# Kernel tuning notes

Measured on AMD Instinct MI355X. Metric: run time of the kernel, lower is better.

## Reference

```python
import jax, jax.numpy as jnp
import numpy as np

D_MODEL, DFF, OUT, SEQ = 256, 1024, 32, 512
SIGMA = 0.1          # sigma for q/k/v/z SMC noise
SIGMA_OBS = 0.5      # observation noise


def _layernorm(x, g, b, eps=1e-6):
    mu = jnp.mean(x, axis=-1, keepdims=True)
    var = jnp.mean(jnp.square(x - mu), axis=-1, keepdims=True)
    return (x - mu) * jax.lax.rsqrt(var + eps) * g + b


def _resample(params, i_t, t):
    # params: (B,P,S,D); i_t: (B,P) ancestor indices; resample only the past [:t+1]
    past = jnp.take_along_axis(params[:, :, :t + 1, :], i_t[:, :, None, None], axis=1)
    return jnp.concatenate([past, params[:, :, t + 1:, :]], axis=2)


def setup_inputs() -> dict:
    key = jax.random.key(0)
    ks = jax.random.split(key, 24)
    B, P = 32, 10
    d = {
        'x': jax.random.normal(ks[0], (B, P, D_MODEL), jnp.float32),
        'y': jax.random.normal(ks[1], (B, P, OUT), jnp.float32),
        'K': jax.random.normal(ks[2], (B, P, SEQ, D_MODEL), jnp.float32),
        'V': jax.random.normal(ks[3], (B, P, SEQ, D_MODEL), jnp.float32),
        'R': jax.random.normal(ks[4], (B, P, SEQ, D_MODEL), jnp.float32),
        'noise_q': jax.random.normal(ks[5], (B, P, 1, D_MODEL), jnp.float32),
        'noise_k': jax.random.normal(ks[6], (B, P, 1, D_MODEL), jnp.float32),
        'noise_v': jax.random.normal(ks[7], (B, P, 1, D_MODEL), jnp.float32),
        'noise_z': jax.random.normal(ks[8], (B, P, 1, D_MODEL), jnp.float32),
        'dec_timestep': 256,
    }
    s = 0.02
    d['wq_w'] = jax.random.normal(ks[9], (D_MODEL, D_MODEL), jnp.float32) * s
    d['wq_b'] = jnp.zeros((D_MODEL,), jnp.float32)
    d['wk_w'] = jax.random.normal(ks[10], (D_MODEL, D_MODEL), jnp.float32) * s
    d['wk_b'] = jnp.zeros((D_MODEL,), jnp.float32)
    d['wv_w'] = jax.random.normal(ks[11], (D_MODEL, D_MODEL), jnp.float32) * s
    d['wv_b'] = jnp.zeros((D_MODEL,), jnp.float32)
    d['wz_w'] = jax.random.normal(ks[12], (D_MODEL, D_MODEL), jnp.float32) * s
    d['wz_b'] = jnp.zeros((D_MODEL,), jnp.float32)
    d['ln1_g'] = jnp.ones((D_MODEL,), jnp.float32)
    d['ln1_b'] = jnp.zeros((D_MODEL,), jnp.float32)
    d['ffn_w1'] = jax.random.normal(ks[13], (D_MODEL, DFF), jnp.float32) * s
    d['ffn_b1'] = jnp.zeros((DFF,), jnp.float32)
    d['ffn_w2'] = jax.random.normal(ks[14], (DFF, D_MODEL), jnp.float32) * s
    d['ffn_b2'] = jnp.zeros((D_MODEL,), jnp.float32)
    d['ln2_g'] = jnp.ones((D_MODEL,), jnp.float32)
    d['ln2_b'] = jnp.zeros((D_MODEL,), jnp.float32)
    d['out_w'] = jax.random.normal(ks[15], (D_MODEL, OUT), jnp.float32) * s
    d['out_b'] = jnp.zeros((OUT,), jnp.float32)
    return d


def reference(x, y, K, V, R, noise_q, noise_k, noise_v, noise_z,
              wq_w, wq_b, wk_w, wk_b, wv_w, wv_b, wz_w, wz_b,
              ln1_g, ln1_b, ffn_w1, ffn_b1, ffn_w2, ffn_b2,
              ln2_g, ln2_b, out_w, out_b, dec_timestep):
    t = dec_timestep
    B, P, D = x.shape
    sq = jnp.sqrt(jnp.float32(SIGMA))
    xq = x[:, :, None, :]           # (B,P,1,D)
    yq = y[:, :, None, :]           # (B,P,1,F_y)
    # --- Self_Attention_SMC: project current token, add SMC gaussian noise ---
    q = xq @ wq_w + wq_b + sq * noise_q
    k = xq @ wk_w + wk_b + sq * noise_k
    v = xq @ wv_w + wv_b + sq * noise_v
    # in-place style KV cache update at timestep t (concat past/new/future)
    K = jnp.concatenate([K[:, :, :t, :], k, K[:, :, t + 1:, :]], axis=2)
    V = jnp.concatenate([V[:, :, :t, :], v, V[:, :, t + 1:, :]], axis=2)
    logits = jnp.einsum('bpod,bpsd->bpos', q, K) / jnp.sqrt(jnp.float32(D))
    attn_weights = jax.nn.softmax(logits, axis=-1)          # (B,P,1,S)
    z = jnp.einsum('bpos,bpsd->bpod', attn_weights, V)
    z = z @ wz_w + wz_b + sq * noise_z
    # --- full_model: layernorm + FFN + layernorm ---
    out = _layernorm(z + xq, ln1_g, ln1_b)
    r = jax.nn.relu(out @ ffn_w1 + ffn_b1) @ ffn_w2 + ffn_b2
    r = _layernorm(r + out, ln2_g, ln2_b)                   # (B,P,1,D)
    predictions = r @ out_w + out_b                          # (B,P,1,F_y)
    R = jnp.concatenate([R[:, :, :t, :], r, R[:, :, t + 1:, :]], axis=2)
    mu = jnp.squeeze(yq - predictions, axis=-2)              # (B,P,F_y)
    log_w = -jnp.sum(mu * mu, axis=-1) / (2.0 * SIGMA_OBS)   # (B,P)
    w = jax.nn.softmax(jnp.exp(log_w), axis=-1)              # faithful to original (softmax of exp)
    w = jax.lax.stop_gradient(w)
    # categorical resampling of ancestors (tf.random.categorical uses w as logits)
    i_t = jax.random.categorical(jax.random.key(42), w[:, None, :], shape=(B, P))
    i_t = jax.lax.stop_gradient(i_t)
    K = _resample(K, i_t, t)
    V = _resample(V, i_t, t)
    R = _resample(R, i_t, t)
    return r, attn_weights, K, V, R, w
```

## Files before the change

kernel.cpp:

```cpp
#include <hip/hip_runtime.h>
#include <hip/hip_bf16.h>
#include <stdint.h>

#define BATCH 32
#define NPART 10
#define BP_TOT 320
#define DM 256
#define FF 1024
#define OD 32
#define SL 512

#define SQRT_SIGMA 0.31622776601683794f

__device__ __forceinline__ uint32_t rotl32(uint32_t x, uint32_t r) {
    return (x << r) | (x >> (32u - r));
}

__device__ __forceinline__ void threefry2x32(uint32_t k0, uint32_t k1,
                                             uint32_t x0, uint32_t x1,
                                             uint32_t& o0, uint32_t& o1) {
    uint32_t k2 = k0 ^ k1 ^ 0x1BD11BDAu;
    uint32_t x = x0 + k0, y = x1 + k1;
#define TFR(r) { x += y; y = rotl32(y, r); y ^= x; }
    TFR(13u) TFR(15u) TFR(26u) TFR(6u)
    x += k1; y += k2 + 1u;
    TFR(17u) TFR(29u) TFR(16u) TFR(24u)
    x += k2; y += k0 + 2u;
    TFR(13u) TFR(15u) TFR(26u) TFR(6u)
    x += k0; y += k1 + 3u;
    TFR(17u) TFR(29u) TFR(16u) TFR(24u)
    x += k1; y += k2 + 4u;
    TFR(13u) TFR(15u) TFR(26u) TFR(6u)
    x += k2; y += k0 + 5u;
#undef TFR
    o0 = x; o1 = y;
}

__device__ __forceinline__ float jax_gumbel_part(uint32_t m) {
    const float TINY = 1.17549435e-38f;
    uint32_t o0, o1;
    threefry2x32(0u, 42u, 0u, m, o0, o1);
    uint32_t bits = o0 ^ o1;
    uint32_t fb = (bits >> 9) | 0x3f800000u;
    float f = __uint_as_float(fb) - 1.0f;
    float u = fmaxf(TINY, f + TINY);
    return -logf(-logf(u));
}

__global__ __launch_bounds__(256) void qkv_kernel(
    const float* __restrict__ x,
    const float* __restrict__ nq, const float* __restrict__ nk,
    const float* __restrict__ nv,
    const float* __restrict__ wq_w, const float* __restrict__ wq_b,
    const float* __restrict__ wk_w, const float* __restrict__ wk_b,
    const float* __restrict__ wv_w, const float* __restrict__ wv_b,
    float* __restrict__ qtmp, float* __restrict__ knew, float* __restrict__ vnew)
{
    const int bp = blockIdx.x;
    const int m  = blockIdx.y;
    const int d  = threadIdx.x;

    __shared__ float xs[DM];
    xs[d] = x[bp * DM + d];
    __syncthreads();

    const float* W; const float* bias; const float* noise; float* outp;
    if (m == 0)      { W = wq_w; bias = wq_b; noise = nq; outp = qtmp + (size_t)bp * SL; }
    else if (m == 1) { W = wk_w; bias = wk_b; noise = nk; outp = knew + (size_t)bp * DM; }
    else             { W = wv_w; bias = wv_b; noise = nv; outp = vnew + (size_t)bp * DM; }

    float a0 = 0.f, a1 = 0.f, a2 = 0.f, a3 = 0.f;
    #pragma unroll 4
    for (int i = 0; i < 64; ++i) {
        a0 = fmaf(xs[i],       W[(i      ) * DM + d], a0);
        a1 = fmaf(xs[i +  64], W[(i +  64) * DM + d], a1);
        a2 = fmaf(xs[i + 128], W[(i + 128) * DM + d], a2);
        a3 = fmaf(xs[i + 192], W[(i + 192) * DM + d], a3);
    }
    outp[d] = (a0 + a1) + (a2 + a3) + bias[d] + SQRT_SIGMA * noise[bp * DM + d];
}

__global__ __launch_bounds__(256) void attn_chunk_kernel(
    const float* __restrict__ Kin, const float* __restrict__ Vin,
    const float* __restrict__ knew, const float* __restrict__ vnew,
    const float* __restrict__ qtmp, const int* __restrict__ t_ptr,
    float* __restrict__ Kout, float* __restrict__ Vout,
    float* __restrict__ logits, float* __restrict__ zpart,
    float* __restrict__ mstat)
{
    const int bp   = blockIdx.x;
    const int sc   = blockIdx.y;
    const int tid  = threadIdx.x;
    const int lane = tid & 63;
    const int wave = tid >> 6;
    const int t    = *t_ptr;

    __shared__ float qs[DM], ks[DM], vs[DM];
    __shared__ float att_loc[128];
    __shared__ float scratch[4 * 256];
    __shared__ float redm[2], rede[2];

    if (tid < DM) {
        qs[tid] = qtmp[(size_t)bp * SL + tid];
        ks[tid] = knew[(size_t)bp * DM + tid];
        vs[tid] = vnew[(size_t)bp * DM + tid];
    }
    __syncthreads();

    const float* Kbp = Kin + (size_t)bp * SL * DM;
    const float* Vbp = Vin + (size_t)bp * SL * DM;
    float4 q4 = *(const float4*)&qs[lane * 4];
    const int s0 = sc * 128 + wave * 32;

    for (int j0 = 0; j0 < 32; j0 += 8) {
        float4 k4[8];
        #pragma unroll
        for (int u = 0; u < 8; ++u) {
            int s = s0 + j0 + u;
            k4[u] = (s == t) ? *(const float4*)&ks[lane * 4]
                             : *(const float4*)&Kbp[(size_t)s * DM + lane * 4];
        }
        #pragma unroll
        for (int u = 0; u < 8; ++u) {
            int s = s0 + j0 + u;
            if (s > t) *(float4*)(Kout + ((size_t)bp * SL + s) * DM + lane * 4) = k4[u];
            float acc = q4.x * k4[u].x + q4.y * k4[u].y + q4.z * k4[u].z + q4.w * k4[u].w;
            #pragma unroll
            for (int off = 32; off; off >>= 1) acc += __shfl_down(acc, off);
            if (lane == 0) {
                float l = acc * 0.0625f;
                att_loc[wave * 32 + j0 + u] = l;
                logits[(size_t)bp * SL + s] = l;
            }
        }
    }
    __syncthreads();

    float l = (tid < 128) ? att_loc[tid] : -3.402823466e+38f;
    float mm = l;
    #pragma unroll
    for (int off = 32; off; off >>= 1) mm = fmaxf(mm, __shfl_down(mm, off));
    if (tid < 128 && lane == 0) redm[wave] = mm;
    __syncthreads();
    const float m_loc = fmaxf(redm[0], redm[1]);
    float p = (tid < 128) ? expf(l - m_loc) : 0.f;
    if (tid < 128) att_loc[tid] = p;
    float e = p;
    #pragma unroll
    for (int off = 32; off; off >>= 1) e += __shfl_down(e, off);
    if (tid < 128 && lane == 0) rede[wave] = e;
    __syncthreads();
    const float e_loc = rede[0] + rede[1];

    float4 z4 = make_float4(0.f, 0.f, 0.f, 0.f);
    for (int j0 = 0; j0 < 32; j0 += 8) {
        float4 v4[8];
        #pragma unroll
        for (int u = 0; u < 8; ++u) {
            int s = s0 + j0 + u;
            v4[u] = (s == t) ? *(const float4*)&vs[lane * 4]
                             : *(const float4*)&Vbp[(size_t)s * DM + lane * 4];
        }
        #pragma unroll
        for (int u = 0; u < 8; ++u) {
            int s = s0 + j0 + u;
            if (s > t) *(float4*)(Vout + ((size_t)bp * SL + s) * DM + lane * 4) = v4[u];
            float a = att_loc[wave * 32 + j0 + u];
            z4.x = fmaf(a, v4[u].x, z4.x);
            z4.y = fmaf(a, v4[u].y, z4.y);
            z4.z = fmaf(a, v4[u].z, z4.z);
            z4.w = fmaf(a, v4[u].w, z4.w);
        }
    }
    *(float4*)&scratch[wave * 256 + lane * 4] = z4;
    __syncthreads();
    if (tid < DM) {
        float zp = (scratch[tid] + scratch[256 + tid]) + (scratch[512 + tid] + scratch[768 + tid]);
        zpart[((size_t)bp * 4 + sc) * DM + tid] = zp;
    }
    if (tid == 0) {
        mstat[((size_t)bp * 4 + sc) * 2 + 0] = m_loc;
        mstat[((size_t)bp * 4 + sc) * 2 + 1] = e_loc;
    }
}

__global__ __launch_bounds__(256) void attn_combine_kernel(
    const float* __restrict__ logits, const float* __restrict__ zpart,
    const float* __restrict__ mstat,
    float* __restrict__ attn_out, float* __restrict__ ztmp)
{
    const int bp  = blockIdx.x;
    const int tid = threadIdx.x;

    const float* ms = mstat + (size_t)bp * 8;
    float m0 = ms[0], e0 = ms[1], m1 = ms[2], e1 = ms[3];
    float m2 = ms[4], e2 = ms[5], m3 = ms[6], e3 = ms[7];
    float gm = fmaxf(fmaxf(m0, m1), fmaxf(m2, m3));
    float f0 = expf(m0 - gm), f1 = expf(m1 - gm);
    float f2 = expf(m2 - gm), f3 = expf(m3 - gm);
    float inv = 1.0f / (e0 * f0 + e1 * f1 + e2 * f2 + e3 * f3);

    float l0 = logits[(size_t)bp * SL + tid];
    float l1 = logits[(size_t)bp * SL + tid + 256];
    attn_out[(size_t)bp * SL + tid]       = expf(l0 - gm) * inv;
    attn_out[(size_t)bp * SL + tid + 256] = expf(l1 - gm) * inv;

    const float* zp = zpart + (size_t)bp * 4 * DM;
    float z = (zp[tid] * f0 + zp[DM + tid] * f1)
            + (zp[2 * DM + tid] * f2 + zp[3 * DM + tid] * f3);
    ztmp[(size_t)bp * DM + tid] = z * inv;
}

__global__ __launch_bounds__(1024) void post_kernel(
    const float* __restrict__ x, const float* __restrict__ nz,
    const float* __restrict__ wz_w, const float* __restrict__ wz_b,
    const float* __restrict__ ln1_g, const float* __restrict__ ln1_b,
    const float* __restrict__ w1, const float* __restrict__ b1,
    const float* __restrict__ w2, const float* __restrict__ b2,
    const float* __restrict__ ln2_g, const float* __restrict__ ln2_b,
    float* __restrict__ r_out)
{
    const int bp   = blockIdx.x;
    const int tid  = threadIdx.x;
    const int lane = tid & 63;
    const int wave = tid >> 6;
    const int grp  = tid >> 8;
    const int qtid = tid & 255;

    __shared__ float buf[DM];
    __shared__ float xs[DM];
    __shared__ float hid[FF];
    __shared__ float scratch[1024];
    __shared__ float red[32];

    if (tid < DM) {
        buf[tid] = r_out[(size_t)bp * DM + tid];
        xs[tid]  = x[bp * DM + tid];
    }
    __syncthreads();

    {
        const int i0 = grp * 64;
        float a0 = 0.f, a1 = 0.f;
        #pragma unroll 4
        for (int ii = 0; ii < 32; ++ii) {
            a0 = fmaf(buf[i0 + ii],      wz_w[(i0 + ii)      * DM + qtid], a0);
            a1 = fmaf(buf[i0 + ii + 32], wz_w[(i0 + ii + 32) * DM + qtid], a1);
        }
        scratch[grp * 256 + qtid] = a0 + a1;
    }
    __syncthreads();
    float h = 0.f;
    if (tid < DM) {
        float az = (scratch[tid] + scratch[256 + tid]) + (scratch[512 + tid] + scratch[768 + tid]);
        h = az + wz_b[tid] + SQRT_SIGMA * nz[bp * DM + tid] + xs[tid];
    }

    float s1 = h;
    #pragma unroll
    for (int off = 32; off; off >>= 1) s1 += __shfl_down(s1, off);
    if (lane == 0) red[wave] = s1;
    __syncthreads();
    float mu = (red[0] + red[1] + red[2] + red[3]) * (1.0f / DM);
    float dv = (tid < DM) ? (h - mu) : 0.f;
    float s2 = dv * dv;
    #pragma unroll
    for (int off = 32; off; off >>= 1) s2 += __shfl_down(s2, off);
    if (lane == 0) red[16 + wave] = s2;
    __syncthreads();
    float var = (red[16] + red[17] + red[18] + red[19]) * (1.0f / DM);
    float o = 0.f;
    __syncthreads();
    if (tid < DM) {
        o = dv * rsqrtf(var + 1e-6f) * ln1_g[tid] + ln1_b[tid];
        buf[tid] = o;
    }
    __syncthreads();

    {
        float h0 = 0.f, h1 = 0.f, h2 = 0.f, h3 = 0.f;
        #pragma unroll 4
        for (int i = 0; i < 64; ++i) {
            h0 = fmaf(buf[i],       w1[(i      ) * FF + tid], h0);
            h1 = fmaf(buf[i +  64], w1[(i +  64) * FF + tid], h1);
            h2 = fmaf(buf[i + 128], w1[(i + 128) * FF + tid], h2);
            h3 = fmaf(buf[i + 192], w1[(i + 192) * FF + tid], h3);
        }
        hid[tid] = fmaxf((h0 + h1) + (h2 + h3) + b1[tid], 0.f);
    }
    __syncthreads();

    {
        const int i0 = grp * 256;
        float a0 = 0.f, a1 = 0.f, a2 = 0.f, a3 = 0.f;
        #pragma unroll 4
        for (int ii = 0; ii < 64; ++ii) {
            a0 = fmaf(hid[i0 + ii],       w2[(i0 + ii      ) * DM + qtid], a0);
            a1 = fmaf(hid[i0 + ii +  64], w2[(i0 + ii +  64) * DM + qtid], a1);
            a2 = fmaf(hid[i0 + ii + 128], w2[(i0 + ii + 128) * DM + qtid], a2);
            a3 = fmaf(hid[i0 + ii + 192], w2[(i0 + ii + 192) * DM + qtid], a3);
        }
        scratch[grp * 256 + qtid] = (a0 + a1) + (a2 + a3);
    }
    __syncthreads();
    float rr = 0.f;
    if (tid < DM) {
        rr = (scratch[tid] + scratch[256 + tid]) + (scratch[512 + tid] + scratch[768 + tid])
           + b2[tid] + o;
    }

    float t1 = rr;
    #pragma unroll
    for (int off = 32; off; off >>= 1) t1 += __shfl_down(t1, off);
    if (lane == 0) red[wave] = t1;
    __syncthreads();
    float mu2 = (red[0] + red[1] + red[2] + red[3]) * (1.0f / DM);
    float dv2 = (tid < DM) ? (rr - mu2) : 0.f;
    float t2 = dv2 * dv2;
    #pragma unroll
    for (int off = 32; off; off >>= 1) t2 += __shfl_down(t2, off);
    if (lane == 0) red[16 + wave] = t2;
    __syncthreads();
    float var2 = (red[16] + red[17] + red[18] + red[19]) * (1.0f / DM);
    if (tid < DM) {
        float rf = dv2 * rsqrtf(var2 + 1e-6f) * ln2_g[tid] + ln2_b[tid];
        r_out[(size_t)bp * DM + tid] = rf;
    }
}

__global__ __launch_bounds__(320) void weights_kernel(
    const float* __restrict__ r, const float* __restrict__ y,
    const float* __restrict__ out_w, const float* __restrict__ out_b,
    float* __restrict__ w_out, int* __restrict__ i_t)
{
    const int b   = blockIdx.x;
    const int tid = threadIdx.x;
    const int p   = tid >> 5;
    const int j   = tid & 31;

    __shared__ float sred[NPART];
    __shared__ float es[NPART];
    __shared__ float pe[NPART];
    __shared__ float wsm[NPART];

    const float* rrow = r + (size_t)(b * NPART + p) * DM;
    float acc = 0.f;
    #pragma unroll 4
    for (int i = 0; i < DM; ++i) acc = fmaf(rrow[i], out_w[i * OD + j], acc);
    float pred = acc + out_b[j];
    float muv  = y[(size_t)(b * NPART + p) * OD + j] - pred;
    float s    = muv * muv;
    #pragma unroll
    for (int off = 16; off; off >>= 1) s += __shfl_down(s, off, 32);
    if (j == 0) sred[p] = s;
    __syncthreads();

    if (tid < NPART) es[tid] = expf(-sred[tid]);
    __syncthreads();
    if (tid < NPART) {
        float mx = es[0];
        #pragma unroll
        for (int i = 1; i < NPART; ++i) mx = fmaxf(mx, es[i]);
        pe[tid] = expf(es[tid] - mx);
    }
    __syncthreads();
    if (tid < NPART) {
        float sum = 0.f;
        #pragma unroll
        for (int i = 0; i < NPART; ++i) sum += pe[i];
        float wv = pe[tid] / sum;
        w_out[b * NPART + tid] = wv;
        wsm[tid] = wv;
    }
    __syncthreads();

    if (tid < NPART) {
        int pp = tid;
        int best = 0;
        float bests = -3.402823466e+38f;
        #pragma unroll
        for (int jj = 0; jj < NPART; ++jj) {
            uint32_t m = (uint32_t)(b * 100 + pp * 10 + jj);
            float score = jax_gumbel_part(m) + wsm[jj];
            if (score > bests) { bests = score; best = jj; }
        }
        i_t[b * NPART + pp] = best;
    }
}

__global__ __launch_bounds__(256) void resample_kernel(
    const float* __restrict__ Kin, const float* __restrict__ Vin,
    const float* __restrict__ Rin,
    const float* __restrict__ knew, const float* __restrict__ vnew,
    const float* __restrict__ rnew,
    const int* __restrict__ i_t, const int* __restrict__ t_ptr,
    float* __restrict__ Kout, float* __restrict__ Vout, float* __restrict__ Rout)
{
    const int t    = *t_ptr;
    const int ysel = blockIdx.y;
    const int tid  = threadIdx.x;
    size_t idx  = (size_t)blockIdx.x * 256 + tid;
    int lane4 = (int)(idx & 63);
    int row   = (int)(idx >> 6);
    int bpi   = row >> 9;
    int s     = row & 511;

    if (ysel != 2 && s > t) return;

    int b     = bpi / NPART;
    int p     = bpi - b * NPART;
    int srcp  = (s <= t) ? i_t[bpi] : p;
    int src_bpi = b * NPART + srcp;

    const float* src;
    if (s == t) {
        const float* nb = (ysel == 1) ? knew : (ysel == 0) ? vnew : rnew;
        src = nb + (size_t)src_bpi * DM;
    } else {
        const float* base = (ysel == 1) ? Kin : (ysel == 0) ? Vin : Rin;
        src = base + ((size_t)src_bpi * SL + s) * DM;
    }
    float* outb = (ysel == 1) ? Kout : (ysel == 0) ? Vout : Rout;
    float4 v4 = *(const float4*)(src + (size_t)lane4 * 4);
    *(float4*)(outb + (size_t)row * DM + (size_t)lane4 * 4) = v4;
}

extern "C" void kernel_launch(void* const* d_in, const int* in_sizes, int n_in,
                              void* d_out, int out_size, void* d_ws, size_t ws_size,
                              hipStream_t stream) {
    const float* x    = (const float*)d_in[0];
    const float* y    = (const float*)d_in[1];
    const float* Kin  = (const float*)d_in[2];
    const float* Vin  = (const float*)d_in[3];
    const float* Rin  = (const float*)d_in[4];
    const float* nq   = (const float*)d_in[5];
    const float* nk   = (const float*)d_in[6];
    const float* nv   = (const float*)d_in[7];
    const float* nz   = (const float*)d_in[8];
    const int*   tptr = (const int*)d_in[9];
    const float* wq_w = (const float*)d_in[10];
    const float* wq_b = (const float*)d_in[11];
    const float* wk_w = (const float*)d_in[12];
    const float* wk_b = (const float*)d_in[13];
    const float* wv_w = (const float*)d_in[14];
    const float* wv_b = (const float*)d_in[15];
    const float* wz_w = (const float*)d_in[16];
    const float* wz_b = (const float*)d_in[17];
    const float* ln1g = (const float*)d_in[18];
    const float* ln1b = (const float*)d_in[19];
    const float* w1   = (const float*)d_in[20];
    const float* b1   = (const float*)d_in[21];
    const float* w2   = (const float*)d_in[22];
    const float* b2   = (const float*)d_in[23];
    const float* ln2g = (const float*)d_in[24];
    const float* ln2b = (const float*)d_in[25];
    const float* outw = (const float*)d_in[26];
    const float* outb = (const float*)d_in[27];

    float* out = (float*)d_out;
    const size_t R_ELEMS    = (size_t)BP_TOT * DM;
    const size_t ATTN_ELEMS = (size_t)BP_TOT * SL;
    const size_t KVR_ELEMS  = (size_t)BP_TOT * SL * DM;
    float* r_out    = out;
    float* attn_out = out + R_ELEMS;
    float* K_out    = out + R_ELEMS + ATTN_ELEMS;
    float* V_out    = K_out + KVR_ELEMS;
    float* R_out    = V_out + KVR_ELEMS;
    float* w_out    = R_out + KVR_ELEMS;

    float* knew = (float*)d_ws;
    float* vnew = knew + R_ELEMS;
    int*   i_t  = (int*)(vnew + R_ELEMS);

    float* logits = R_out;
    float* zpart  = R_out + ATTN_ELEMS;
    float* mstat  = zpart + (size_t)BP_TOT * 4 * DM;

    qkv_kernel<<<dim3(BP_TOT, 3), 256, 0, stream>>>(
        x, nq, nk, nv, wq_w, wq_b, wk_w, wk_b, wv_w, wv_b,
        attn_out, knew, vnew);

    attn_chunk_kernel<<<dim3(BP_TOT, 4), 256, 0, stream>>>(
        Kin, Vin, knew, vnew, attn_out, tptr,
        K_out, V_out, logits, zpart, mstat);

    attn_combine_kernel<<<BP_TOT, 256, 0, stream>>>(
        logits, zpart, mstat, attn_out, r_out);

    post_kernel<<<BP_TOT, 1024, 0, stream>>>(
        x, nz, wz_w, wz_b, ln1g, ln1b, w1, b1, w2, b2, ln2g, ln2b,
        r_out);

    weights_kernel<<<BATCH, 320, 0, stream>>>(
        r_out, y, outw, outb, w_out, i_t);

    resample_kernel<<<dim3(163840 / 4, 3), 256, 0, stream>>>(
        Kin, Vin, Rin, knew, vnew, r_out, i_t, tptr,
        K_out, V_out, R_out);
}
```

Baseline: 337.8 us.

## Batch four particles per block in QKV and post kernels, fuse attention combine

The QKV projection and the post-attention FFN kernels now each handle four particle rows per block, so every weight element loaded from memory feeds four FMAs instead of one. The separate attention-combine kernel is folded into the start of the post kernel, which removes one launch and the round trip of the combined z vector through global memory. Per-thread reductions become longer (full 256- or 1024-deep dot products), and the grids shrink to 80 blocks, which may leave many compute units idle. Shared memory use per block grows as well.

```diff
diff --git a/kernel.cpp b/kernel.cpp
--- a/kernel.cpp
+++ b/kernel.cpp
@@ -56,28 +56,38 @@
     const float* __restrict__ wv_w, const float* __restrict__ wv_b,
     float* __restrict__ qtmp, float* __restrict__ knew, float* __restrict__ vnew)
 {
-    const int bp = blockIdx.x;
+    const int bb = blockIdx.x;
     const int m  = blockIdx.y;
     const int d  = threadIdx.x;
 
-    __shared__ float xs[DM];
-    xs[d] = x[bp * DM + d];
-    __syncthreads();
-
-    const float* W; const float* bias; const float* noise; float* outp;
-    if (m == 0)      { W = wq_w; bias = wq_b; noise = nq; outp = qtmp + (size_t)bp * SL; }
-    else if (m == 1) { W = wk_w; bias = wk_b; noise = nk; outp = knew + (size_t)bp * DM; }
-    else             { W = wv_w; bias = wv_b; noise = nv; outp = vnew + (size_t)bp * DM; }
+    __shared__ float xs[4][DM];
+    #pragma unroll
+    for (int g = 0; g < 4; ++g) xs[g][d] = x[(bb * 4 + g) * DM + d];
+    __syncthreads();
+
+    const float* W; const float* bias; const float* noise;
+    if (m == 0)      { W = wq_w; bias = wq_b; noise = nq; }
+    else if (m == 1) { W = wk_w; bias = wk_b; noise = nk; }
+    else             { W = wv_w; bias = wv_b; noise = nv; }
 
     float a0 = 0.f, a1 = 0.f, a2 = 0.f, a3 = 0.f;
     #pragma unroll 4
-    for (int i = 0; i < 64; ++i) {
-        a0 = fmaf(xs[i],       W[(i      ) * DM + d], a0);
-        a1 = fmaf(xs[i +  64], W[(i +  64) * DM + d], a1);
-        a2 = fmaf(xs[i + 128], W[(i + 128) * DM + d], a2);
-        a3 = fmaf(xs[i + 192], W[(i + 192) * DM + d], a3);
-    }
-    outp[d] = (a0 + a1) + (a2 + a3) + bias[d] + SQRT_SIGMA * noise[bp * DM + d];
+    for (int i = 0; i < DM; ++i) {
+        float wv = W[i * DM + d];
+        a0 = fmaf(xs[0][i], wv, a0);
+        a1 = fmaf(xs[1][i], wv, a1);
+        a2 = fmaf(xs[2][i], wv, a2);
+        a3 = fmaf(xs[3][i], wv, a3);
+    }
+    float r[4] = {a0, a1, a2, a3};
+    #pragma unroll
+    for (int g = 0; g < 4; ++g) {
+        int bp = bb * 4 + g;
+        float v = r[g] + bias[d] + SQRT_SIGMA * noise[bp * DM + d];
+        if (m == 0)      qtmp[(size_t)bp * SL + d] = v;
+        else if (m == 1) knew[(size_t)bp * DM + d] = v;
+        else             vnew[(size_t)bp * DM + d] = v;
+    }
 }
 
 __global__ __launch_bounds__(256) void attn_chunk_kernel(
@@ -184,148 +194,127 @@
     }
 }
 
-__global__ __launch_bounds__(256) void attn_combine_kernel(
+__global__ __launch_bounds__(1024) void post_kernel(
+    const float* __restrict__ x, const float* __restrict__ nz,
     const float* __restrict__ logits, const float* __restrict__ zpart,
     const float* __restrict__ mstat,
-    float* __restrict__ attn_out, float* __restrict__ ztmp)
-{
-    const int bp  = blockIdx.x;
-    const int tid = threadIdx.x;
-
-    const float* ms = mstat + (size_t)bp * 8;
-    float m0 = ms[0], e0 = ms[1], m1 = ms[2], e1 = ms[3];
-    float m2 = ms[4], e2 = ms[5], m3 = ms[6], e3 = ms[7];
-    float gm = fmaxf(fmaxf(m0, m1), fmaxf(m2, m3));
-    float f0 = expf(m0 - gm), f1 = expf(m1 - gm);
-    float f2 = expf(m2 - gm), f3 = expf(m3 - gm);
-    float inv = 1.0f / (e0 * f0 + e1 * f1 + e2 * f2 + e3 * f3);
-
-    float l0 = logits[(size_t)bp * SL + tid];
-    float l1 = logits[(size_t)bp * SL + tid + 256];
-    attn_out[(size_t)bp * SL + tid]       = expf(l0 - gm) * inv;
-    attn_out[(size_t)bp * SL + tid + 256] = expf(l1 - gm) * inv;
-
-    const float* zp = zpart + (size_t)bp * 4 * DM;
-    float z = (zp[tid] * f0 + zp[DM + tid] * f1)
-            + (zp[2 * DM + tid] * f2 + zp[3 * DM + tid] * f3);
-    ztmp[(size_t)bp * DM + tid] = z * inv;
-}
-
-__global__ __launch_bounds__(1024) void post_kernel(
-    const float* __restrict__ x, const float* __restrict__ nz,
     const float* __restrict__ wz_w, const float* __restrict__ wz_b,
     const float* __restrict__ ln1_g, const float* __restrict__ ln1_b,
     const float* __restrict__ w1, const float* __restrict__ b1,
     const float* __restrict__ w2, const float* __restrict__ b2,
     const float* __restrict__ ln2_g, const float* __restrict__ ln2_b,
-    float* __restrict__ r_out)
+    float* __restrict__ attn_out, float* __restrict__ r_out)
 {
-    const int bp   = blockIdx.x;
+    const int bb   = blockIdx.x;
     const int tid  = threadIdx.x;
-    const int lane = tid & 63;
-    const int wave = tid >> 6;
-    const int grp  = tid >> 8;
-    const int qtid = tid & 255;
-
-    __shared__ float buf[DM];
-    __shared__ float xs[DM];
-    __shared__ float hid[FF];
-    __shared__ float scratch[1024];
-    __shared__ float red[32];
-
-    if (tid < DM) {
-        buf[tid] = r_out[(size_t)bp * DM + tid];
-        xs[tid]  = x[bp * DM + tid];
-    }
-    __syncthreads();
+    const int g    = tid >> 8;
+    const int d    = tid & 255;
+    const int wg   = (tid >> 6) & 3;
+    const int bp   = bb * 4 + g;
+
+    __shared__ float bufz[4][DM];
+    __shared__ float xs4[4][DM];
+    __shared__ float hid4[4][FF];
+    __shared__ float part[4][4][DM];
+    __shared__ float red2[4][8];
 
     {
-        const int i0 = grp * 64;
-        float a0 = 0.f, a1 = 0.f;
+        const float* ms = mstat + (size_t)bp * 8;
+        float m0 = ms[0], e0 = ms[1], m1 = ms[2], e1 = ms[3];
+        float m2 = ms[4], e2 = ms[5], m3 = ms[6], e3 = ms[7];
+        float gm = fmaxf(fmaxf(m0, m1), fmaxf(m2, m3));
+        float f0 = expf(m0 - gm), f1 = expf(m1 - gm);
+        float f2 = expf(m2 - gm), f3 = expf(m3 - gm);
+        float inv = 1.0f / (e0 * f0 + e1 * f1 + e2 * f2 + e3 * f3);
+
+        const float* zp = zpart + (size_t)bp * 4 * DM;
+        float z = (zp[d] * f0 + zp[DM + d] * f1)
+                + (zp[2 * DM + d] * f2 + zp[3 * DM + d] * f3);
+        bufz[g][d] = z * inv;
+
+        float l0 = logits[(size_t)bp * SL + d];
+        float l1 = logits[(size_t)bp * SL + 256 + d];
+        attn_out[(size_t)bp * SL + d]       = expf(l0 - gm) * inv;
+        attn_out[(size_t)bp * SL + 256 + d] = expf(l1 - gm) * inv;
+        xs4[g][d] = x[bp * DM + d];
+    }
+    __syncthreads();
+
+    float acc = 0.f;
+    #pragma unroll 4
+    for (int i = 0; i < DM; ++i) acc = fmaf(bufz[g][i], wz_w[i * DM + d], acc);
+    float h = acc + wz_b[d] + SQRT_SIGMA * nz[bp * DM + d] + xs4[g][d];
+
+    float s1 = h;
+    #pragma unroll
+    for (int off = 32; off; off >>= 1) s1 += __shfl_down(s1, off);
+    if ((tid & 63) == 0) red2[g][wg] = s1;
+    __syncthreads();
+    float mu = (red2[g][0] + red2[g][1] + red2[g][2] + red2[g][3]) * (1.0f / DM);
+    float dv = h - mu;
+    float s2 = dv * dv;
+    #pragma unroll
+    for (int off = 32; off; off >>= 1) s2 += __shfl_down(s2, off);
+    if ((tid & 63) == 0) red2[g][4 + wg] = s2;
+    __syncthreads();
+    float var = (red2[g][4] + red2[g][5] + red2[g][6] + red2[g][7]) * (1.0f / DM);
+    float o = dv * rsqrtf(var + 1e-6f) * ln1_g[d] + ln1_b[d];
+    __syncthreads();
+    bufz[g][d] = o;
+    __syncthreads();
+
+    {
+        float c0 = 0.f, c1 = 0.f, c2 = 0.f, c3 = 0.f;
         #pragma unroll 4
-        for (int ii = 0; ii < 32; ++ii) {
-            a0 = fmaf(buf[i0 + ii],      wz_w[(i0 + ii)      * DM + qtid], a0);
-            a1 = fmaf(buf[i0 + ii + 32], wz_w[(i0 + ii + 32) * DM + qtid], a1);
-        }
-        scratch[grp * 256 + qtid] = a0 + a1;
-    }
-    __syncthreads();
-    float h = 0.f;
-    if (tid < DM) {
-        float az = (scratch[tid] + scratch[256 + tid]) + (scratch[512 + tid] + scratch[768 + tid]);
-        h = az + wz_b[tid] + SQRT_SIGMA * nz[bp * DM + tid] + xs[tid];
-    }
-
-    float s1 = h;
-    #pragma unroll
-    for (int off = 32; off; off >>= 1) s1 += __shfl_down(s1, off);
-    if (lane == 0) red[wave] = s1;
-    __syncthreads();
-    float mu = (red[0] + red[1] + red[2] + red[3]) * (1.0f / DM);
-    float dv = (tid < DM) ? (h - mu) : 0.f;
-    float s2 = dv * dv;
-    #pragma unroll
-    for (int off = 32; off; off >>= 1) s2 += __shfl_down(s2, off);
-    if (lane == 0) red[16 + wave] = s2;
-    __syncthreads();
-    float var = (red[16] + red[17] + red[18] + red[19]) * (1.0f / DM);
-    float o = 0.f;
-    __syncthreads();
-    if (tid < DM) {
-        o = dv * rsqrtf(var + 1e-6f) * ln1_g[tid] + ln1_b[tid];
-        buf[tid] = o;
+        for (int i = 0; i < DM; ++i) {
+            float wv = w1[i * FF + tid];
+            c0 = fmaf(bufz[0][i], wv, c0);
+            c1 = fmaf(bufz[1][i], wv, c1);
+            c2 = fmaf(bufz[2][i], wv, c2);
+            c3 = fmaf(bufz[3][i], wv, c3);
+        }
+        float bb1 = b1[tid];
+        hid4[0][tid] = fmaxf(c0 + bb1, 0.f);
+        hid4[1][tid] = fmaxf(c1 + bb1, 0.f);
+        hid4[2][tid] = fmaxf(c2 + bb1, 0.f);
+        hid4[3][tid] = fmaxf(c3 + bb1, 0.f);
     }
     __syncthreads();
 
     {
-        float h0 = 0.f, h1 = 0.f, h2 = 0.f, h3 = 0.f;
+        float a0 = 0.f, a1 = 0.f, a2 = 0.f, a3 = 0.f;
+        const int i0 = g * 256;
         #pragma unroll 4
-        for (int i = 0; i < 64; ++i) {
-            h0 = fmaf(buf[i],       w1[(i      ) * FF + tid], h0);
-            h1 = fmaf(buf[i +  64], w1[(i +  64) * FF + tid], h1);
-            h2 = fmaf(buf[i + 128], w1[(i + 128) * FF + tid], h2);
-            h3 = fmaf(buf[i + 192], w1[(i + 192) * FF + tid], h3);
-        }
-        hid[tid] = fmaxf((h0 + h1) + (h2 + h3) + b1[tid], 0.f);
-    }
-    __syncthreads();
-
-    {
-        const int i0 = grp * 256;
-        float a0 = 0.f, a1 = 0.f, a2 = 0.f, a3 = 0.f;
-        #pragma unroll 4
-        for (int ii = 0; ii < 64; ++ii) {
-            a0 = fmaf(hid[i0 + ii],       w2[(i0 + ii      ) * DM + qtid], a0);
-            a1 = fmaf(hid[i0 + ii +  64], w2[(i0 + ii +  64) * DM + qtid], a1);
-            a2 = fmaf(hid[i0 + ii + 128], w2[(i0 + ii + 128) * DM + qtid], a2);
-            a3 = fmaf(hid[i0 + ii + 192], w2[(i0 + ii + 192) * DM + qtid], a3);
-        }
-        scratch[grp * 256 + qtid] = (a0 + a1) + (a2 + a3);
-    }
-    __syncthreads();
-    float rr = 0.f;
-    if (tid < DM) {
-        rr = (scratch[tid] + scratch[256 + tid]) + (scratch[512 + tid] + scratch[768 + tid])
-           + b2[tid] + o;
-    }
+        for (int ii = 0; ii < 256; ++ii) {
+            int i = i0 + ii;
+            float wv = w2[i * DM + d];
+            a0 = fmaf(hid4[0][i], wv, a0);
+            a1 = fmaf(hid4[1][i], wv, a1);
+            a2 = fmaf(hid4[2][i], wv, a2);
+            a3 = fmaf(hid4[3][i], wv, a3);
+        }
+        part[g][0][d] = a0; part[g][1][d] = a1;
+        part[g][2][d] = a2; part[g][3][d] = a3;
+    }
+    __syncthreads();
+    float rr = (part[0][g][d] + part[1][g][d]) + (part[2][g][d] + part[3][g][d])
+             + b2[d] + o;
 
     float t1 = rr;
     #pragma unroll
     for (int off = 32; off; off >>= 1) t1 += __shfl_down(t1, off);
-    if (lane == 0) red[wave] = t1;
-    __syncthreads();
-    float mu2 = (red[0] + red[1] + red[2] + red[3]) * (1.0f / DM);
-    float dv2 = (tid < DM) ? (rr - mu2) : 0.f;
+    if ((tid & 63) == 0) red2[g][wg] = t1;
+    __syncthreads();
+    float mu2 = (red2[g][0] + red2[g][1] + red2[g][2] + red2[g][3]) * (1.0f / DM);
+    float dv2 = rr - mu2;
     float t2 = dv2 * dv2;
     #pragma unroll
     for (int off = 32; off; off >>= 1) t2 += __shfl_down(t2, off);
-    if (lane == 0) red[16 + wave] = t2;
-    __syncthreads();
-    float var2 = (red[16] + red[17] + red[18] + red[19]) * (1.0f / DM);
-    if (tid < DM) {
-        float rf = dv2 * rsqrtf(var2 + 1e-6f) * ln2_g[tid] + ln2_b[tid];
-        r_out[(size_t)bp * DM + tid] = rf;
-    }
+    if ((tid & 63) == 0) red2[g][4 + wg] = t2;
+    __syncthreads();
+    float var2 = (red2[g][4] + red2[g][5] + red2[g][6] + red2[g][7]) * (1.0f / DM);
+    float rf = dv2 * rsqrtf(var2 + 1e-6f) * ln2_g[d] + ln2_b[d];
+    r_out[(size_t)bp * DM + d] = rf;
 }
 
 __global__ __launch_bounds__(320) void weights_kernel(
@@ -476,7 +465,7 @@
     float* zpart  = R_out + ATTN_ELEMS;
     float* mstat  = zpart + (size_t)BP_TOT * 4 * DM;
 
-    qkv_kernel<<<dim3(BP_TOT, 3), 256, 0, stream>>>(
+    qkv_kernel<<<dim3(BP_TOT / 4, 3), 256, 0, stream>>>(
         x, nq, nk, nv, wq_w, wq_b, wk_w, wk_b, wv_w, wv_b,
         attn_out, knew, vnew);
 
@@ -484,12 +473,10 @@
         Kin, Vin, knew, vnew, attn_out, tptr,
         K_out, V_out, logits, zpart, mstat);
 
-    attn_combine_kernel<<<BP_TOT, 256, 0, stream>>>(
-        logits, zpart, mstat, attn_out, r_out);
-
-    post_kernel<<<BP_TOT, 1024, 0, stream>>>(
-        x, nz, wz_w, wz_b, ln1g, ln1b, w1, b1, w2, b2, ln2g, ln2b,
-        r_out);
+    post_kernel<<<BP_TOT / 4, 1024, 0, stream>>>(
+        x, nz, logits, zpart, mstat,
+        wz_w, wz_b, ln1g, ln1b, w1, b1, w2, b2, ln2g, ln2b,
+        attn_out, r_out);
 
     weights_kernel<<<BATCH, 320, 0, stream>>>(
         r_out, y, outw, outb, w_out, i_t);
```

Result: slower. 380.3 us (+12.6%).

## Fuse attention combine into post kernel, split sequence into more chunks, batch QKV

Applied to the files above, without the earlier changes.

Removes the separate attention-combine launch by folding the cross-chunk softmax merge and the z reduction into the start of the post kernel. The attention chunk kernel now splits each sequence into 8 chunks of 64 rows instead of 4 of 128, which doubles the block count for better occupancy on the memory-bound K/V pass. The QKV projection now processes 4 particles per block so each weight load is reused four times. The trade-offs are more partial z/mstat traffic and more blocks repeating the q/k/v shared-memory loads.

```diff
diff --git a/kernel.cpp b/kernel.cpp
--- a/kernel.cpp
+++ b/kernel.cpp
@@ -9,6 +9,8 @@
 #define FF 1024
 #define OD 32
 #define SL 512
+#define NCHUNK 8
+#define CROWS 64
 
 #define SQRT_SIGMA 0.31622776601683794f
 
@@ -56,28 +58,38 @@
     const float* __restrict__ wv_w, const float* __restrict__ wv_b,
     float* __restrict__ qtmp, float* __restrict__ knew, float* __restrict__ vnew)
 {
-    const int bp = blockIdx.x;
+    const int bb = blockIdx.x;
     const int m  = blockIdx.y;
     const int d  = threadIdx.x;
 
-    __shared__ float xs[DM];
-    xs[d] = x[bp * DM + d];
-    __syncthreads();
-
-    const float* W; const float* bias; const float* noise; float* outp;
-    if (m == 0)      { W = wq_w; bias = wq_b; noise = nq; outp = qtmp + (size_t)bp * SL; }
-    else if (m == 1) { W = wk_w; bias = wk_b; noise = nk; outp = knew + (size_t)bp * DM; }
-    else             { W = wv_w; bias = wv_b; noise = nv; outp = vnew + (size_t)bp * DM; }
+    __shared__ float xs[4][DM];
+    #pragma unroll
+    for (int g = 0; g < 4; ++g) xs[g][d] = x[(bb * 4 + g) * DM + d];
+    __syncthreads();
+
+    const float* W; const float* bias; const float* noise;
+    if (m == 0)      { W = wq_w; bias = wq_b; noise = nq; }
+    else if (m == 1) { W = wk_w; bias = wk_b; noise = nk; }
+    else             { W = wv_w; bias = wv_b; noise = nv; }
 
     float a0 = 0.f, a1 = 0.f, a2 = 0.f, a3 = 0.f;
     #pragma unroll 4
-    for (int i = 0; i < 64; ++i) {
-        a0 = fmaf(xs[i],       W[(i      ) * DM + d], a0);
-        a1 = fmaf(xs[i +  64], W[(i +  64) * DM + d], a1);
-        a2 = fmaf(xs[i + 128], W[(i + 128) * DM + d], a2);
-        a3 = fmaf(xs[i + 192], W[(i + 192) * DM + d], a3);
-    }
-    outp[d] = (a0 + a1) + (a2 + a3) + bias[d] + SQRT_SIGMA * noise[bp * DM + d];
+    for (int i = 0; i < DM; ++i) {
+        float wv = W[i * DM + d];
+        a0 = fmaf(xs[0][i], wv, a0);
+        a1 = fmaf(xs[1][i], wv, a1);
+        a2 = fmaf(xs[2][i], wv, a2);
+        a3 = fmaf(xs[3][i], wv, a3);
+    }
+    float r[4] = {a0, a1, a2, a3};
+    #pragma unroll
+    for (int g = 0; g < 4; ++g) {
+        int bp = bb * 4 + g;
+        float v = r[g] + bias[d] + SQRT_SIGMA * noise[bp * DM + d];
+        if (m == 0)      qtmp[(size_t)bp * SL + d] = v;
+        else if (m == 1) knew[(size_t)bp * DM + d] = v;
+        else             vnew[(size_t)bp * DM + d] = v;
+    }
 }
 
 __global__ __launch_bounds__(256) void attn_chunk_kernel(
@@ -96,23 +108,21 @@
     const int t    = *t_ptr;
 
     __shared__ float qs[DM], ks[DM], vs[DM];
-    __shared__ float att_loc[128];
+    __shared__ float att_loc[CROWS];
     __shared__ float scratch[4 * 256];
-    __shared__ float redm[2], rede[2];
-
-    if (tid < DM) {
-        qs[tid] = qtmp[(size_t)bp * SL + tid];
-        ks[tid] = knew[(size_t)bp * DM + tid];
-        vs[tid] = vnew[(size_t)bp * DM + tid];
-    }
+    __shared__ float redm[1], rede[1];
+
+    qs[tid] = qtmp[(size_t)bp * SL + tid];
+    ks[tid] = knew[(size_t)bp * DM + tid];
+    vs[tid] = vnew[(size_t)bp * DM + tid];
     __syncthreads();
 
     const float* Kbp = Kin + (size_t)bp * SL * DM;
     const float* Vbp = Vin + (size_t)bp * SL * DM;
     float4 q4 = *(const float4*)&qs[lane * 4];
-    const int s0 = sc * 128 + wave * 32;
-
-    for (int j0 = 0; j0 < 32; j0 += 8) {
+    const int s0 = sc * CROWS + wave * 16;
+
+    for (int j0 = 0; j0 < 16; j0 += 8) {
         float4 k4[8];
         #pragma unroll
         for (int u = 0; u < 8; ++u) {
@@ -129,31 +139,35 @@
             for (int off = 32; off; off >>= 1) acc += __shfl_down(acc, off);
             if (lane == 0) {
                 float l = acc * 0.0625f;
-                att_loc[wave * 32 + j0 + u] = l;
+                att_loc[wave * 16 + j0 + u] = l;
                 logits[(size_t)bp * SL + s] = l;
             }
         }
     }
     __syncthreads();
 
-    float l = (tid < 128) ? att_loc[tid] : -3.402823466e+38f;
-    float mm = l;
-    #pragma unroll
-    for (int off = 32; off; off >>= 1) mm = fmaxf(mm, __shfl_down(mm, off));
-    if (tid < 128 && lane == 0) redm[wave] = mm;
-    __syncthreads();
-    const float m_loc = fmaxf(redm[0], redm[1]);
-    float p = (tid < 128) ? expf(l - m_loc) : 0.f;
-    if (tid < 128) att_loc[tid] = p;
-    float e = p;
-    #pragma unroll
-    for (int off = 32; off; off >>= 1) e += __shfl_down(e, off);
-    if (tid < 128 && lane == 0) rede[wave] = e;
-    __syncthreads();
-    const float e_loc = rede[0] + rede[1];
+    if (wave == 0) {
+        float l = att_loc[lane];
+        float mm = l;
+        #pragma unroll
+        for (int off = 32; off; off >>= 1) mm = fmaxf(mm, __shfl_down(mm, off));
+        if (lane == 0) redm[0] = mm;
+    }
+    __syncthreads();
+    const float m_loc = redm[0];
+    if (wave == 0) {
+        float p = expf(att_loc[lane] - m_loc);
+        att_loc[lane] = p;
+        float e = p;
+        #pragma unroll
+        for (int off = 32; off; off >>= 1) e += __shfl_down(e, off);
+        if (lane == 0) rede[0] = e;
+    }
+    __syncthreads();
+    const float e_loc = rede[0];
 
     float4 z4 = make_float4(0.f, 0.f, 0.f, 0.f);
-    for (int j0 = 0; j0 < 32; j0 += 8) {
+    for (int j0 = 0; j0 < 16; j0 += 8) {
         float4 v4[8];
         #pragma unroll
         for (int u = 0; u < 8; ++u) {
@@ -165,7 +179,7 @@
         for (int u = 0; u < 8; ++u) {
             int s = s0 + j0 + u;
             if (s > t) *(float4*)(Vout + ((size_t)bp * SL + s) * DM + lane * 4) = v4[u];
-            float a = att_loc[wave * 32 + j0 + u];
+            float a = att_loc[wave * 16 + j0 + u];
             z4.x = fmaf(a, v4[u].x, z4.x);
             z4.y = fmaf(a, v4[u].y, z4.y);
             z4.z = fmaf(a, v4[u].z, z4.z);
@@ -176,49 +190,24 @@
     __syncthreads();
     if (tid < DM) {
         float zp = (scratch[tid] + scratch[256 + tid]) + (scratch[512 + tid] + scratch[768 + tid]);
-        zpart[((size_t)bp * 4 + sc) * DM + tid] = zp;
+        zpart[((size_t)bp * NCHUNK + sc) * DM + tid] = zp;
     }
     if (tid == 0) {
-        mstat[((size_t)bp * 4 + sc) * 2 + 0] = m_loc;
-        mstat[((size_t)bp * 4 + sc) * 2 + 1] = e_loc;
-    }
-}
-
-__global__ __launch_bounds__(256) void attn_combine_kernel(
+        mstat[((size_t)bp * NCHUNK + sc) * 2 + 0] = m_loc;
+        mstat[((size_t)bp * NCHUNK + sc) * 2 + 1] = e_loc;
+    }
+}
+
+__global__ __launch_bounds__(1024) void post_kernel(
+    const float* __restrict__ x, const float* __restrict__ nz,
     const float* __restrict__ logits, const float* __restrict__ zpart,
     const float* __restrict__ mstat,
-    float* __restrict__ attn_out, float* __restrict__ ztmp)
-{
-    const int bp  = blockIdx.x;
-    const int tid = threadIdx.x;
-
-    const float* ms = mstat + (size_t)bp * 8;
-    float m0 = ms[0], e0 = ms[1], m1 = ms[2], e1 = ms[3];
-    float m2 = ms[4], e2 = ms[5], m3 = ms[6], e3 = ms[7];
-    float gm = fmaxf(fmaxf(m0, m1), fmaxf(m2, m3));
-    float f0 = expf(m0 - gm), f1 = expf(m1 - gm);
-    float f2 = expf(m2 - gm), f3 = expf(m3 - gm);
-    float inv = 1.0f / (e0 * f0 + e1 * f1 + e2 * f2 + e3 * f3);
-
-    float l0 = logits[(size_t)bp * SL + tid];
-    float l1 = logits[(size_t)bp * SL + tid + 256];
-    attn_out[(size_t)bp * SL + tid]       = expf(l0 - gm) * inv;
-    attn_out[(size_t)bp * SL + tid + 256] = expf(l1 - gm) * inv;
-
-    const float* zp = zpart + (size_t)bp * 4 * DM;
-    float z = (zp[tid] * f0 + zp[DM + tid] * f1)
-            + (zp[2 * DM + tid] * f2 + zp[3 * DM + tid] * f3);
-    ztmp[(size_t)bp * DM + tid] = z * inv;
-}
-
-__global__ __launch_bounds__(1024) void post_kernel(
-    const float* __restrict__ x, const float* __restrict__ nz,
     const float* __restrict__ wz_w, const float* __restrict__ wz_b,
     const float* __restrict__ ln1_g, const float* __restrict__ ln1_b,
     const float* __restrict__ w1, const float* __restrict__ b1,
     const float* __restrict__ w2, const float* __restrict__ b2,
     const float* __restrict__ ln2_g, const float* __restrict__ ln2_b,
-    float* __restrict__ r_out)
+    float* __restrict__ attn_out, float* __restrict__ r_out)
 {
     const int bp   = blockIdx.x;
     const int tid  = threadIdx.x;
@@ -233,9 +222,35 @@
     __shared__ float scratch[1024];
     __shared__ float red[32];
 
-    if (tid < DM) {
-        buf[tid] = r_out[(size_t)bp * DM + tid];
-        xs[tid]  = x[bp * DM + tid];
+    const float* ms = mstat + (size_t)bp * (2 * NCHUNK);
+    float mc[NCHUNK], ec[NCHUNK];
+    float gm = -3.402823466e+38f;
+    #pragma unroll
+    for (int c = 0; c < NCHUNK; ++c) {
+        mc[c] = ms[2 * c]; ec[c] = ms[2 * c + 1];
+        gm = fmaxf(gm, mc[c]);
+    }
+    float fc[NCHUNK], denom = 0.f;
+    #pragma unroll
+    for (int c = 0; c < NCHUNK; ++c) {
+        fc[c] = expf(mc[c] - gm);
+        denom = fmaf(ec[c], fc[c], denom);
+    }
+    const float inv = 1.0f / denom;
+
+    if (tid < 512) {
+        float l = logits[(size_t)bp * SL + tid];
+        attn_out[(size_t)bp * SL + tid] = expf(l - gm) * inv;
+    } else if (tid < 768) {
+        int d = tid - 512;
+        const float* zp = zpart + (size_t)bp * NCHUNK * DM;
+        float z = 0.f;
+        #pragma unroll
+        for (int c = 0; c < NCHUNK; ++c) z = fmaf(zp[c * DM + d], fc[c], z);
+        buf[d] = z * inv;
+    } else {
+        int d = tid - 768;
+        xs[d] = x[bp * DM + d];
     }
     __syncthreads();
 
@@ -474,22 +489,20 @@
 
     float* logits = R_out;
     float* zpart  = R_out + ATTN_ELEMS;
-    float* mstat  = zpart + (size_t)BP_TOT * 4 * DM;
-
-    qkv_kernel<<<dim3(BP_TOT, 3), 256, 0, stream>>>(
+    float* mstat  = zpart + (size_t)BP_TOT * NCHUNK * DM;
+
+    qkv_kernel<<<dim3(BP_TOT / 4, 3), 256, 0, stream>>>(
         x, nq, nk, nv, wq_w, wq_b, wk_w, wk_b, wv_w, wv_b,
         attn_out, knew, vnew);
 
-    attn_chunk_kernel<<<dim3(BP_TOT, 4), 256, 0, stream>>>(
+    attn_chunk_kernel<<<dim3(BP_TOT, NCHUNK), 256, 0, stream>>>(
         Kin, Vin, knew, vnew, attn_out, tptr,
         K_out, V_out, logits, zpart, mstat);
 
-    attn_combine_kernel<<<BP_TOT, 256, 0, stream>>>(
-        logits, zpart, mstat, attn_out, r_out);
-
     post_kernel<<<BP_TOT, 1024, 0, stream>>>(
-        x, nz, wz_w, wz_b, ln1g, ln1b, w1, b1, w2, b2, ln2g, ln2b,
-        r_out);
+        x, nz, logits, zpart, mstat,
+        wz_w, wz_b, ln1g, ln1b, w1, b1, w2, b2, ln2g, ln2b,
+        attn_out, r_out);
 
     weights_kernel<<<BATCH, 320, 0, stream>>>(
         r_out, y, outw, outb, w_out, i_t);
```

Result: slower. 346.6 us (+2.6%).
